# Kernel tuning notes

Hardware: AMD Instinct MI355X
Metric: run time of the kernel (lower is better)

Reference implementation:

```python
import jax, jax.numpy as jnp
import numpy as np

N = 8192       # number of nodes (dense NxN attention)
F_IN = 256     # input feature dim
F_OUT = 64     # projected feature dim (F_prime)
NEG_SLOPE = 0.01  # nn.LeakyReLU default


def setup_inputs() -> dict:
    key = jax.random.key(0)
    k0, k1, k2, k3 = jax.random.split(key, 4)
    H = jax.random.normal(k0, (N, F_IN), dtype=jnp.float32)
    # dense 0/1 adjacency; force self-loops so every row has a nonzero denominator
    A = jax.random.randint(k1, (N, N), 0, 2, dtype=jnp.int32)
    A = jnp.maximum(A, jnp.eye(N, dtype=jnp.int32))
    # learned params: W : F_IN -> F_OUT (self.W), a : 2*F_OUT -> 1 (self.a)
    W = jax.random.normal(k2, (F_IN, F_OUT), dtype=jnp.float32) / np.sqrt(F_IN)
    bW = jnp.zeros((F_OUT,), dtype=jnp.float32)
    a_w = jax.random.normal(k3, (2 * F_OUT,), dtype=jnp.float32) / np.sqrt(2 * F_OUT)
    a_b = jnp.zeros((), dtype=jnp.float32)
    return {"H": H, "A": A, "W": W, "bW": bW, "a_w": a_w, "a_b": a_b}


def reference(H, A, W, bW, a_w, a_b):
    # Wh[i] = W(H[i])  -> [N, F_OUT]
    Wh = H @ W + bW
    # a([Wh_i ; Wh_j]) = a1.Wh_i + a2.Wh_j + a_b : decompose the concat-linear
    s_src = Wh @ a_w[:F_OUT]           # [N]
    s_tar = Wh @ a_w[F_OUT:]           # [N]
    logits = s_src[:, None] + s_tar[None, :] + a_b   # [N, N]
    # e_ij = exp(leaky_relu(logits))
    e = jnp.exp(jnp.where(logits >= 0, logits, NEG_SLOPE * logits))
    # denominator masks by adjacency (sum_j e_ij * A_ij), as in the original
    denom = jnp.sum(e * A.astype(e.dtype), axis=1, keepdims=True)  # [N, 1]
    alpha = e / denom                   # NOTE: numerator NOT masked (faithful)
    # H'_i = sigmoid(alpha_i @ Wh)
    return jax.nn.sigmoid(alpha @ Wh)   # [N, F_OUT]
```

## Files before the change

### kernel.cpp

```cpp
#include <hip/hip_runtime.h>
#include <hip/hip_bf16.h>

#define NN 8192
#define FIN 256
#define FOUT 64

__global__ __launch_bounds__(256) void k1_proj(
    const float* __restrict__ H, const float* __restrict__ W,
    const float* __restrict__ bW, const float* __restrict__ aw,
    const float* __restrict__ ab,
    float* __restrict__ Wh, float* __restrict__ s_src, float* __restrict__ t_tar,
    float* __restrict__ E1, float* __restrict__ E2, float* __restrict__ PP)
{
    __shared__ float Hs[16 * FIN];
    int tid = threadIdx.x;
    int i0 = blockIdx.x * 16;
    const float4* Hv = (const float4*)(H + (size_t)i0 * FIN);
    float4* Hsv = (float4*)Hs;
    for (int idx = tid; idx < 16 * FIN / 4; idx += 256) Hsv[idx] = Hv[idx];
    __syncthreads();
    int f = tid & 63, sub = tid >> 6;
    float a1f = aw[f], a2f = aw[64 + f];
    float b = bW[f];
    float acc0 = b, acc1 = b, acc2 = b, acc3 = b;
    for (int k = 0; k < FIN; ++k) {
        float w = W[k * FOUT + f];
        acc0 += Hs[(sub     ) * FIN + k] * w;
        acc1 += Hs[(sub +  4) * FIN + k] * w;
        acc2 += Hs[(sub +  8) * FIN + k] * w;
        acc3 += Hs[(sub + 12) * FIN + k] * w;
    }
    float accs[4] = {acc0, acc1, acc2, acc3};
    #pragma unroll
    for (int q = 0; q < 4; ++q) {
        int i = i0 + sub + 4 * q;
        float a = accs[q];
        Wh[(size_t)i * FOUT + f] = a;
        float v1 = a * a1f, v2 = a * a2f;
        #pragma unroll
        for (int o = 32; o > 0; o >>= 1) {
            v1 += __shfl_xor(v1, o);
            v2 += __shfl_xor(v2, o);
        }
        if (f == 0) {
            float s = v1 + ab[0];
            float t = v2;
            s_src[i] = s; t_tar[i] = t;
            E1[i] = __expf(s); E2[i] = __expf(0.01f * s);
            PP[2 * i]     = __expf(t);
            PP[2 * i + 1] = __expf(0.01f * t);
        }
    }
}

__global__ __launch_bounds__(256) void k2_rank(
    const float* __restrict__ t_tar, const float* __restrict__ s_src,
    int* __restrict__ sorted_idx, int* __restrict__ kidx)
{
    __shared__ float Ts[NN];
    int tid = threadIdx.x;
    const float4* tv = (const float4*)t_tar;
    float4* Tsv = (float4*)Ts;
    for (int idx = tid; idx < NN / 4; idx += 256) Tsv[idx] = tv[idx];
    __syncthreads();
    int wv = tid >> 6, lane = tid & 63;
    int g = blockIdx.x * 4 + wv;
    float tj = Ts[g];
    float thr = -s_src[g];
    int rank = 0, kc = 0;
    #pragma unroll 4
    for (int k = lane; k < NN; k += 64) {
        float tk = Ts[k];
        rank += (tk < tj || (tk == tj && k < g)) ? 1 : 0;
        kc   += (tk < thr) ? 1 : 0;
    }
    #pragma unroll
    for (int o = 32; o > 0; o >>= 1) {
        rank += __shfl_xor(rank, o);
        kc   += __shfl_xor(kc, o);
    }
    if (lane == 0) { sorted_idx[rank] = g; kidx[g] = kc; }
}

__global__ __launch_bounds__(64) void k3a_tots(
    const float* __restrict__ Wh, const float* __restrict__ PP,
    const int* __restrict__ sorted_idx,
    float* __restrict__ tots1, float* __restrict__ tots2)
{
    int c = blockIdx.x, f = threadIdx.x;
    float t1 = 0.f, t2 = 0.f;
    int m0 = c * 32;
    #pragma unroll 8
    for (int m = m0; m < m0 + 32; ++m) {
        int sj = sorted_idx[m];
        float wh = Wh[(size_t)sj * 64 + f];
        t1 += PP[2 * sj]     * wh;
        t2 += PP[2 * sj + 1] * wh;
    }
    tots1[c * 64 + f] = t1; tots2[c * 64 + f] = t2;
}

__global__ __launch_bounds__(1024) void k3b_scan(
    const float* __restrict__ tots1, const float* __restrict__ tots2,
    float* __restrict__ off1, float* __restrict__ off2,
    float* __restrict__ pre2, float* __restrict__ suf1)
{
    __shared__ float w1[16 * 64], w2[16 * 64];
    int tid = threadIdx.x, f = tid & 63, wv = tid >> 6;
    int c0 = wv * 16;
    float s1 = 0.f, s2 = 0.f;
    for (int c = c0; c < c0 + 16; ++c) { s1 += tots1[c * 64 + f]; s2 += tots2[c * 64 + f]; }
    w1[wv * 64 + f] = s1; w2[wv * 64 + f] = s2;
    __syncthreads();
    float o2 = 0.f;
    #pragma unroll
    for (int w = 0; w < 16; ++w) if (w < wv) o2 += w2[w * 64 + f];
    float run2 = o2;
    for (int c = c0; c < c0 + 16; ++c) { off2[c * 64 + f] = run2; run2 += tots2[c * 64 + f]; }
    if (wv == 15) pre2[(size_t)NN * 64 + f] = run2;
    float o1 = 0.f;
    #pragma unroll
    for (int w = 0; w < 16; ++w) if (w > wv) o1 += w1[w * 64 + f];
    float run1 = o1;
    for (int c = c0 + 15; c >= c0; --c) { off1[c * 64 + f] = run1; run1 += tots1[c * 64 + f]; }
    if (tid < 64) suf1[(size_t)NN * 64 + tid] = 0.f;
}

__global__ __launch_bounds__(64) void k3c_emit(
    const float* __restrict__ Wh, const float* __restrict__ PP,
    const int* __restrict__ sorted_idx,
    const float* __restrict__ off1, const float* __restrict__ off2,
    float* __restrict__ pre2, float* __restrict__ suf1)
{
    int c = blockIdx.x, f = threadIdx.x;
    int m0 = c * 32;
    float whr[32], p1r[32], p2r[32];
    #pragma unroll
    for (int q = 0; q < 32; ++q) {
        int sj = sorted_idx[m0 + q];
        whr[q] = Wh[(size_t)sj * 64 + f];
        p1r[q] = PP[2 * sj]; p2r[q] = PP[2 * sj + 1];
    }
    float run2 = off2[c * 64 + f];
    #pragma unroll
    for (int q = 0; q < 32; ++q) {
        pre2[(size_t)(m0 + q) * 64 + f] = run2;
        run2 += p2r[q] * whr[q];
    }
    float run1 = off1[c * 64 + f];
    #pragma unroll
    for (int q = 31; q >= 0; --q) {
        run1 += p1r[q] * whr[q];
        suf1[(size_t)(m0 + q) * 64 + f] = run1;
    }
}

__global__ __launch_bounds__(256) void k4_denom(
    const int* __restrict__ A, const float* __restrict__ PP,
    const float* __restrict__ E1, const float* __restrict__ E2,
    float* __restrict__ denom)
{
    __shared__ float red[8];
    int tid = threadIdx.x;
    int i = blockIdx.x;
    float e1 = E1[i];
    float accA = 0.f, accB = 0.f;
    const float4* PPv = (const float4*)PP;
    const int4* Av = (const int4*)(A + (size_t)i * NN);
    #pragma unroll 2
    for (int jv = tid; jv < NN / 4; jv += 256) {
        int4 a4 = Av[jv];
        float4 ppA = PPv[2 * jv];
        float4 ppB = PPv[2 * jv + 1];
        {
            bool c = e1 * ppA.x >= 1.0f;
            float af = (float)a4.x;
            accA += af * (c ? ppA.x : 0.0f);
            accB += af * (c ? 0.0f : ppA.y);
        }
        {
            bool c = e1 * ppA.z >= 1.0f;
            float af = (float)a4.y;
            accA += af * (c ? ppA.z : 0.0f);
            accB += af * (c ? 0.0f : ppA.w);
        }
        {
            bool c = e1 * ppB.x >= 1.0f;
            float af = (float)a4.z;
            accA += af * (c ? ppB.x : 0.0f);
            accB += af * (c ? 0.0f : ppB.y);
        }
        {
            bool c = e1 * ppB.z >= 1.0f;
            float af = (float)a4.w;
            accA += af * (c ? ppB.z : 0.0f);
            accB += af * (c ? 0.0f : ppB.w);
        }
    }
    #pragma unroll
    for (int o = 32; o > 0; o >>= 1) {
        accA += __shfl_xor(accA, o);
        accB += __shfl_xor(accB, o);
    }
    int wv = tid >> 6;
    if ((tid & 63) == 0) { red[wv * 2] = accA; red[wv * 2 + 1] = accB; }
    __syncthreads();
    if (tid == 0) {
        float sA = red[0] + red[2] + red[4] + red[6];
        float sB = red[1] + red[3] + red[5] + red[7];
        denom[i] = e1 * sA + E2[i] * sB;
    }
}

__global__ __launch_bounds__(256) void k5_out(
    const float* __restrict__ suf1, const float* __restrict__ pre2,
    const int* __restrict__ kidx, const float* __restrict__ E1,
    const float* __restrict__ E2, const float* __restrict__ denom,
    float* __restrict__ out)
{
    int tid = threadIdx.x;
    int f = tid & 63, sub = tid >> 6;
    int i = blockIdx.x * 4 + sub;
    int k = kidx[i];
    float num = E1[i] * suf1[(size_t)k * 64 + f] + E2[i] * pre2[(size_t)k * 64 + f];
    float x = num / denom[i];
    out[(size_t)i * 64 + f] = 1.0f / (1.0f + __expf(-x));
}

extern "C" void kernel_launch(void* const* d_in, const int* in_sizes, int n_in,
                              void* d_out, int out_size, void* d_ws, size_t ws_size,
                              hipStream_t stream) {
    const float* H  = (const float*)d_in[0];
    const int*   A  = (const int*)d_in[1];
    const float* W  = (const float*)d_in[2];
    const float* bW = (const float*)d_in[3];
    const float* aw = (const float*)d_in[4];
    const float* ab = (const float*)d_in[5];
    float* out = (float*)d_out;

    float* ws    = (float*)d_ws;
    float* Wh    = ws;
    float* s_src = Wh + 524288;
    float* t_tar = s_src + 8192;
    float* E1    = t_tar + 8192;
    float* E2    = E1 + 8192;
    float* PP    = E2 + 8192;
    float* denom = PP + 16384;
    float* pre2  = denom + 8192;
    float* suf1  = pre2 + 524352;
    float* tots1 = suf1 + 524352;
    float* tots2 = tots1 + 16384;
    float* off1  = tots2 + 16384;
    float* off2  = off1 + 16384;
    int* sorted_idx = (int*)(off2 + 16384);
    int* kidx       = sorted_idx + 8192;

    hipLaunchKernelGGL(k1_proj, dim3(512), dim3(256), 0, stream,
                       H, W, bW, aw, ab, Wh, s_src, t_tar, E1, E2, PP);
    hipLaunchKernelGGL(k2_rank, dim3(2048), dim3(256), 0, stream,
                       t_tar, s_src, sorted_idx, kidx);
    hipLaunchKernelGGL(k3a_tots, dim3(256), dim3(64), 0, stream,
                       Wh, PP, sorted_idx, tots1, tots2);
    hipLaunchKernelGGL(k3b_scan, dim3(1), dim3(1024), 0, stream,
                       tots1, tots2, off1, off2, pre2, suf1);
    hipLaunchKernelGGL(k3c_emit, dim3(256), dim3(64), 0, stream,
                       Wh, PP, sorted_idx, off1, off2, pre2, suf1);
    hipLaunchKernelGGL(k4_denom, dim3(8192), dim3(256), 0, stream,
                       A, PP, E1, E2, denom);
    hipLaunchKernelGGL(k5_out, dim3(2048), dim3(256), 0, stream,
                       suf1, pre2, kidx, E1, E2, denom, out);
}
```

Baseline: 424.7 us.

## Precompute attention scores via folded weights and merge projection, rank, denom into one launch

Scores s and t are now computed directly from H using W·a folded into two 256-vectors, so the projection no longer gates the score stage. The Wh projection, the rank/count sort and the adjacency-masked denominator then run as disjoint block ranges of a single launch, overlapping compute-bound work with the bandwidth-bound read of A. The rank stage handles eight targets per wave and reads t from global memory instead of staging it in LDS. A is loaded with nontemporal hints to avoid polluting cache. The risks are the extra pass over H, slight floating-point differences from the folded dot products, and uneven block workloads inside the merged kernel.

New measurement: 419.2 us. No clear change (-1.3%).

```diff
diff --git a/kernel.cpp b/kernel.cpp
--- a/kernel.cpp
+++ b/kernel.cpp
@@ -5,46 +5,56 @@
 #define FIN 256
 #define FOUT 64
 
-__global__ __launch_bounds__(256) void k1_proj(
+typedef int iv4 __attribute__((ext_vector_type(4)));
+
+__global__ __launch_bounds__(256) void k0_st(
     const float* __restrict__ H, const float* __restrict__ W,
     const float* __restrict__ bW, const float* __restrict__ aw,
     const float* __restrict__ ab,
-    float* __restrict__ Wh, float* __restrict__ s_src, float* __restrict__ t_tar,
+    float* __restrict__ s_src, float* __restrict__ t_tar,
     float* __restrict__ E1, float* __restrict__ E2, float* __restrict__ PP)
 {
-    __shared__ float Hs[16 * FIN];
+    __shared__ float us[FIN], vs[FIN];
     int tid = threadIdx.x;
-    int i0 = blockIdx.x * 16;
-    const float4* Hv = (const float4*)(H + (size_t)i0 * FIN);
-    float4* Hsv = (float4*)Hs;
-    for (int idx = tid; idx < 16 * FIN / 4; idx += 256) Hsv[idx] = Hv[idx];
+    float u = 0.f, v = 0.f;
+    const float4* Wv = (const float4*)(W + tid * FOUT);
+    #pragma unroll
+    for (int fq = 0; fq < FOUT / 4; ++fq) {
+        float4 w4  = Wv[fq];
+        float4 a14 = ((const float4*)aw)[fq];
+        float4 a24 = ((const float4*)(aw + FOUT))[fq];
+        u += w4.x * a14.x + w4.y * a14.y + w4.z * a14.z + w4.w * a14.w;
+        v += w4.x * a24.x + w4.y * a24.y + w4.z * a24.z + w4.w * a24.w;
+    }
+    us[tid] = u; vs[tid] = v;
+    float cb1 = ab[0], cb2 = 0.f;
+    #pragma unroll 8
+    for (int f = 0; f < FOUT; ++f) {
+        float bwf = bW[f];
+        cb1 += bwf * aw[f];
+        cb2 += bwf * aw[FOUT + f];
+    }
     __syncthreads();
-    int f = tid & 63, sub = tid >> 6;
-    float a1f = aw[f], a2f = aw[64 + f];
-    float b = bW[f];
-    float acc0 = b, acc1 = b, acc2 = b, acc3 = b;
-    for (int k = 0; k < FIN; ++k) {
-        float w = W[k * FOUT + f];
-        acc0 += Hs[(sub     ) * FIN + k] * w;
-        acc1 += Hs[(sub +  4) * FIN + k] * w;
-        acc2 += Hs[(sub +  8) * FIN + k] * w;
-        acc3 += Hs[(sub + 12) * FIN + k] * w;
-    }
-    float accs[4] = {acc0, acc1, acc2, acc3};
+    int lane = tid & 63, wv = tid >> 6;
+    int i0 = blockIdx.x * 16 + wv * 4;
     #pragma unroll
     for (int q = 0; q < 4; ++q) {
-        int i = i0 + sub + 4 * q;
-        float a = accs[q];
-        Wh[(size_t)i * FOUT + f] = a;
-        float v1 = a * a1f, v2 = a * a2f;
+        int i = i0 + q;
+        const float* Hr = H + (size_t)i * FIN;
+        float sv = 0.f, tv = 0.f;
+        #pragma unroll
+        for (int m = 0; m < 4; ++m) {
+            float h = Hr[m * 64 + lane];
+            sv += h * us[m * 64 + lane];
+            tv += h * vs[m * 64 + lane];
+        }
         #pragma unroll
         for (int o = 32; o > 0; o >>= 1) {
-            v1 += __shfl_xor(v1, o);
-            v2 += __shfl_xor(v2, o);
-        }
-        if (f == 0) {
-            float s = v1 + ab[0];
-            float t = v2;
+            sv += __shfl_xor(sv, o);
+            tv += __shfl_xor(tv, o);
+        }
+        if (lane == 0) {
+            float s = sv + cb1, t = tv + cb2;
             s_src[i] = s; t_tar[i] = t;
             E1[i] = __expf(s); E2[i] = __expf(0.01f * s);
             PP[2 * i]     = __expf(t);
@@ -53,33 +63,123 @@
     }
 }
 
-__global__ __launch_bounds__(256) void k2_rank(
+__global__ __launch_bounds__(256) void k_mega(
+    const float* __restrict__ H, const float* __restrict__ W,
+    const float* __restrict__ bW,
+    const int* __restrict__ A, const float* __restrict__ PP,
+    const float* __restrict__ E1, const float* __restrict__ E2,
     const float* __restrict__ t_tar, const float* __restrict__ s_src,
+    float* __restrict__ Wh, float* __restrict__ denom,
     int* __restrict__ sorted_idx, int* __restrict__ kidx)
 {
-    __shared__ float Ts[NN];
+    __shared__ float sh[16 * FIN];
     int tid = threadIdx.x;
-    const float4* tv = (const float4*)t_tar;
-    float4* Tsv = (float4*)Ts;
-    for (int idx = tid; idx < NN / 4; idx += 256) Tsv[idx] = tv[idx];
-    __syncthreads();
-    int wv = tid >> 6, lane = tid & 63;
-    int g = blockIdx.x * 4 + wv;
-    float tj = Ts[g];
-    float thr = -s_src[g];
-    int rank = 0, kc = 0;
-    #pragma unroll 4
-    for (int k = lane; k < NN; k += 64) {
-        float tk = Ts[k];
-        rank += (tk < tj || (tk == tj && k < g)) ? 1 : 0;
-        kc   += (tk < thr) ? 1 : 0;
-    }
-    #pragma unroll
-    for (int o = 32; o > 0; o >>= 1) {
-        rank += __shfl_xor(rank, o);
-        kc   += __shfl_xor(kc, o);
-    }
-    if (lane == 0) { sorted_idx[rank] = g; kidx[g] = kc; }
+    int b = blockIdx.x;
+    if (b < 512) {
+        int i0 = b * 16;
+        const float4* Hv = (const float4*)(H + (size_t)i0 * FIN);
+        float4* shv = (float4*)sh;
+        for (int idx = tid; idx < 16 * FIN / 4; idx += 256) shv[idx] = Hv[idx];
+        __syncthreads();
+        int f = tid & 63, sub = tid >> 6;
+        float bb = bW[f];
+        float acc0 = bb, acc1 = bb, acc2 = bb, acc3 = bb;
+        for (int k = 0; k < FIN; ++k) {
+            float w = W[k * FOUT + f];
+            acc0 += sh[(sub     ) * FIN + k] * w;
+            acc1 += sh[(sub +  4) * FIN + k] * w;
+            acc2 += sh[(sub +  8) * FIN + k] * w;
+            acc3 += sh[(sub + 12) * FIN + k] * w;
+        }
+        Wh[(size_t)(i0 + sub     ) * FOUT + f] = acc0;
+        Wh[(size_t)(i0 + sub +  4) * FOUT + f] = acc1;
+        Wh[(size_t)(i0 + sub +  8) * FOUT + f] = acc2;
+        Wh[(size_t)(i0 + sub + 12) * FOUT + f] = acc3;
+    } else if (b < 768) {
+        int rb = b - 512;
+        int lane = tid & 63, wv = tid >> 6;
+        int g0 = rb * 32 + wv * 8;
+        float tj[8], thr[8];
+        int rank[8], kc[8];
+        #pragma unroll
+        for (int q = 0; q < 8; ++q) {
+            tj[q] = t_tar[g0 + q]; thr[q] = -s_src[g0 + q];
+            rank[q] = 0; kc[q] = 0;
+        }
+        for (int k = lane; k < NN; k += 64) {
+            float tk = t_tar[k];
+            #pragma unroll
+            for (int q = 0; q < 8; ++q) {
+                int g = g0 + q;
+                rank[q] += (tk < tj[q] || (tk == tj[q] && k < g)) ? 1 : 0;
+                kc[q]   += (tk < thr[q]) ? 1 : 0;
+            }
+        }
+        #pragma unroll
+        for (int q = 0; q < 8; ++q) {
+            #pragma unroll
+            for (int o = 32; o > 0; o >>= 1) {
+                rank[q] += __shfl_xor(rank[q], o);
+                kc[q]   += __shfl_xor(kc[q], o);
+            }
+        }
+        if (lane == 0) {
+            #pragma unroll
+            for (int q = 0; q < 8; ++q) {
+                sorted_idx[rank[q]] = g0 + q;
+                kidx[g0 + q] = kc[q];
+            }
+        }
+    } else {
+        int i = b - 768;
+        float e1 = E1[i];
+        float accA = 0.f, accB = 0.f;
+        const float4* PPv = (const float4*)PP;
+        const iv4* Av = (const iv4*)(A + (size_t)i * NN);
+        #pragma unroll 2
+        for (int jv = tid; jv < NN / 4; jv += 256) {
+            iv4 a4 = __builtin_nontemporal_load(Av + jv);
+            float4 ppA = PPv[2 * jv];
+            float4 ppB = PPv[2 * jv + 1];
+            {
+                bool c = e1 * ppA.x >= 1.0f;
+                float af = (float)a4.x;
+                accA += af * (c ? ppA.x : 0.0f);
+                accB += af * (c ? 0.0f : ppA.y);
+            }
+            {
+                bool c = e1 * ppA.z >= 1.0f;
+                float af = (float)a4.y;
+                accA += af * (c ? ppA.z : 0.0f);
+                accB += af * (c ? 0.0f : ppA.w);
+            }
+            {
+                bool c = e1 * ppB.x >= 1.0f;
+                float af = (float)a4.z;
+                accA += af * (c ? ppB.x : 0.0f);
+                accB += af * (c ? 0.0f : ppB.y);
+            }
+            {
+                bool c = e1 * ppB.z >= 1.0f;
+                float af = (float)a4.w;
+                accA += af * (c ? ppB.z : 0.0f);
+                accB += af * (c ? 0.0f : ppB.w);
+            }
+        }
+        #pragma unroll
+        for (int o = 32; o > 0; o >>= 1) {
+            accA += __shfl_xor(accA, o);
+            accB += __shfl_xor(accB, o);
+        }
+        int wv = tid >> 6;
+        if ((tid & 63) == 0) { sh[wv * 2] = accA; sh[wv * 2 + 1] = accB; }
+        __syncthreads();
+        if (tid == 0) {
+            float sA = sh[0] + sh[2] + sh[4] + sh[6];
+            float sB = sh[1] + sh[3] + sh[5] + sh[7];
+            denom[i] = e1 * sA + E2[i] * sB;
+        }
+    }
 }
 
 __global__ __launch_bounds__(64) void k3a_tots(
@@ -152,63 +252,6 @@
     for (int q = 31; q >= 0; --q) {
         run1 += p1r[q] * whr[q];
         suf1[(size_t)(m0 + q) * 64 + f] = run1;
-    }
-}
-
-__global__ __launch_bounds__(256) void k4_denom(
-    const int* __restrict__ A, const float* __restrict__ PP,
-    const float* __restrict__ E1, const float* __restrict__ E2,
-    float* __restrict__ denom)
-{
-    __shared__ float red[8];
-    int tid = threadIdx.x;
-    int i = blockIdx.x;
-    float e1 = E1[i];
-    float accA = 0.f, accB = 0.f;
-    const float4* PPv = (const float4*)PP;
-    const int4* Av = (const int4*)(A + (size_t)i * NN);
-    #pragma unroll 2
-    for (int jv = tid; jv < NN / 4; jv += 256) {
-        int4 a4 = Av[jv];
-        float4 ppA = PPv[2 * jv];
-        float4 ppB = PPv[2 * jv + 1];
-        {
-            bool c = e1 * ppA.x >= 1.0f;
-            float af = (float)a4.x;
-            accA += af * (c ? ppA.x : 0.0f);
-            accB += af * (c ? 0.0f : ppA.y);
-        }
-        {
-            bool c = e1 * ppA.z >= 1.0f;
-            float af = (float)a4.y;
-            accA += af * (c ? ppA.z : 0.0f);
-            accB += af * (c ? 0.0f : ppA.w);
-        }
-        {
-            bool c = e1 * ppB.x >= 1.0f;
-            float af = (float)a4.z;
-            accA += af * (c ? ppB.x : 0.0f);
-            accB += af * (c ? 0.0f : ppB.y);
-        }
-        {
-            bool c = e1 * ppB.z >= 1.0f;
-            float af = (float)a4.w;
-            accA += af * (c ? ppB.z : 0.0f);
-            accB += af * (c ? 0.0f : ppB.w);
-        }
-    }
-    #pragma unroll
-    for (int o = 32; o > 0; o >>= 1) {
-        accA += __shfl_xor(accA, o);
-        accB += __shfl_xor(accB, o);
-    }
-    int wv = tid >> 6;
-    if ((tid & 63) == 0) { red[wv * 2] = accA; red[wv * 2 + 1] = accB; }
-    __syncthreads();
-    if (tid == 0) {
-        float sA = red[0] + red[2] + red[4] + red[6];
-        float sB = red[1] + red[3] + red[5] + red[7];
-        denom[i] = e1 * sA + E2[i] * sB;
     }
 }
 
@@ -255,18 +298,17 @@
     int* sorted_idx = (int*)(off2 + 16384);
     int* kidx       = sorted_idx + 8192;
 
-    hipLaunchKernelGGL(k1_proj, dim3(512), dim3(256), 0, stream,
-                       H, W, bW, aw, ab, Wh, s_src, t_tar, E1, E2, PP);
-    hipLaunchKernelGGL(k2_rank, dim3(2048), dim3(256), 0, stream,
-                       t_tar, s_src, sorted_idx, kidx);
+    hipLaunchKernelGGL(k0_st, dim3(512), dim3(256), 0, stream,
+                       H, W, bW, aw, ab, s_src, t_tar, E1, E2, PP);
+    hipLaunchKernelGGL(k_mega, dim3(8960), dim3(256), 0, stream,
+                       H, W, bW, A, PP, E1, E2, t_tar, s_src,
+                       Wh, denom, sorted_idx, kidx);
     hipLaunchKernelGGL(k3a_tots, dim3(256), dim3(64), 0, stream,
                        Wh, PP, sorted_idx, tots1, tots2);
     hipLaunchKernelGGL(k3b_scan, dim3(1), dim3(1024), 0, stream,
                        tots1, tots2, off1, off2, pre2, suf1);
     hipLaunchKernelGGL(k3c_emit, dim3(256), dim3(64), 0, stream,
                        Wh, PP, sorted_idx, off1, off2, pre2, suf1);
-    hipLaunchKernelGGL(k4_denom, dim3(8192), dim3(256), 0, stream,
-                       A, PP, E1, E2, denom);
     hipLaunchKernelGGL(k5_out, dim3(2048), dim3(256), 0, stream,
                        suf1, pre2, kidx, E1, E2, denom, out);
 }
```
